# Optimization experiments

Hardware: AMD Instinct MI355X
Metric: run time of the kernel (lower is better)

The kernel has to match this reference:

```python
import jax, jax.numpy as jnp
import numpy as np
import math

NEG_INF = -1e29
B, L, H = 16, 1024, 512
D = 2 * H          # feature dim of s and q
GELU_C = math.sqrt(2.0 / math.pi)


def gelu(x):
    return 0.5 * x * (1.0 + jnp.tanh(GELU_C * (x + 0.044715 * x ** 3)))


def mask_softmax(W, m1, m2):
    # joint mask: [B, len1, 1] * [B, 1, len2]
    m = (m1[:, :, None] * m2[:, None, :]).astype(W.dtype)
    return jax.nn.softmax(W + (1.0 - m) * NEG_INF, axis=-1)


def heuristic(x, y, w_r, b_r, w_g, b_g):
    inp = jnp.concatenate([x, y, x * y, x - y], axis=-1)  # [B, L, 8H]
    r = gelu(inp @ w_r.T + b_r)                           # [B, L, 2H]
    g = jax.nn.sigmoid(inp @ w_g.T + b_g)
    return g * r + (1.0 - g) * x


def setup_inputs() -> dict:
    key = jax.random.key(0)
    k = jax.random.split(key, 6)
    s = jax.random.normal(k[0], (B, L, D), jnp.float32)
    q = jax.random.normal(k[1], (B, L, D), jnp.float32)
    s_mask = jnp.ones((B, L), jnp.int32)
    q_mask = jnp.ones((B, L), jnp.int32)
    fan_in = 8 * H
    lim = 1.0 / np.sqrt(fan_in)
    w_r = jax.random.uniform(k[2], (2 * H, fan_in), jnp.float32, -lim, lim)
    b_r = jax.random.uniform(k[3], (2 * H,), jnp.float32, -lim, lim)
    w_g = jax.random.uniform(k[4], (2 * H, fan_in), jnp.float32, -lim, lim)
    b_g = jax.random.uniform(k[5], (2 * H,), jnp.float32, -lim, lim)
    return {"s": s, "q": q, "w_r": w_r, "b_r": b_r, "w_g": w_g, "b_g": b_g,
            "s_mask": s_mask, "q_mask": q_mask}


def reference(s, q, w_r, b_r, w_g, b_g, s_mask, q_mask):
    a = jnp.einsum('bsd,btd->bst', s, q)                  # [B, Ls, Lq]
    b = mask_softmax(a, s_mask, q_mask) @ q               # [B, Ls, D]
    c = mask_softmax(a.swapaxes(-1, -2), q_mask, s_mask) @ s  # [B, Lq, D]
    s_tilde = heuristic(s, b, w_r, b_r, w_g, b_g)
    q_tilde = heuristic(q, c, w_r, b_r, w_g, b_g)
    return (s_tilde, q_tilde)
```

## Files before the change

kernel.cpp:

```cpp
#include <hip/hip_runtime.h>
#include <hip/hip_bf16.h>
#include <math.h>

#define DEVI static __device__ __forceinline__

typedef unsigned short u16;
typedef unsigned int u32;
typedef __bf16 bf16_t;
typedef bf16_t bf16x8 __attribute__((ext_vector_type(8)));
typedef float f32x4 __attribute__((ext_vector_type(4)));

static constexpr int Bb = 16;
static constexpr int L  = 1024;
static constexpr int D  = 1024;
static constexpr int KH = 4096;

DEVI u16 f2bf(float f) {
  union { float f; u32 u; } v; v.f = f;
  u32 r = v.u + 0x7FFFu + ((v.u >> 16) & 1u);
  return (u16)(r >> 16);
}

DEVI float bf2f(u16 b) {
  union { u32 u; float f; } v; v.u = ((u32)b) << 16;
  return v.f;
}

DEVI void gload16(const void* g, void* l) {
  __builtin_amdgcn_global_load_lds((const __attribute__((address_space(1))) u32*)g,
                                   (__attribute__((address_space(3))) u32*)l,
                                   16, 0, 0);
}

DEVI int swz(int row, int col) { return col ^ ((row & 7) << 3); }

__global__ void k_cast_split(const float* __restrict__ in, u16* __restrict__ hi,
                             u16* __restrict__ lo, int n4) {
  int i = blockIdx.x * blockDim.x + threadIdx.x;
  int stride = gridDim.x * blockDim.x;
  for (; i < n4; i += stride) {
    float4 v = ((const float4*)in)[i];
    ushort4 h, l;
    h.x = f2bf(v.x); h.y = f2bf(v.y); h.z = f2bf(v.z); h.w = f2bf(v.w);
    l.x = f2bf(v.x - bf2f(h.x));
    l.y = f2bf(v.y - bf2f(h.y));
    l.z = f2bf(v.z - bf2f(h.z));
    l.w = f2bf(v.w - bf2f(h.w));
    ((ushort4*)hi)[i] = h;
    ((ushort4*)lo)[i] = l;
  }
}

__global__ void k_wcat(const float* __restrict__ wr, const float* __restrict__ wg,
                       u16* __restrict__ wcat, int n4) {
  int i = blockIdx.x * blockDim.x + threadIdx.x;
  int stride = gridDim.x * blockDim.x;
  for (; i < n4; i += stride) {
    int j = i >> 10;
    int c4 = i & 1023;
    const float* src = ((j & 1) ? wg : wr) + (size_t)(j >> 1) * 4096 + c4 * 4;
    float4 v = *(const float4*)src;
    ushort4 o;
    o.x = f2bf(v.x); o.y = f2bf(v.y); o.z = f2bf(v.z); o.w = f2bf(v.w);
    ((ushort4*)wcat)[i] = o;
  }
}

__global__ void k_feat(const u16* __restrict__ x, const u16* __restrict__ y,
                       u16* __restrict__ xy, u16* __restrict__ xmy, int n8) {
  int i = blockIdx.x * blockDim.x + threadIdx.x;
  int stride = gridDim.x * blockDim.x;
  for (; i < n8; i += stride) {
    bf16x8 xv = ((const bf16x8*)x)[i];
    bf16x8 yv = ((const bf16x8*)y)[i];
    bf16x8 p, d;
    #pragma unroll
    for (int j = 0; j < 8; ++j) {
      float xf = (float)xv[j], yf = (float)yv[j];
      p[j] = (bf16_t)(xf * yf);
      d[j] = (bf16_t)(xf - yf);
    }
    ((bf16x8*)xy)[i] = p;
    ((bf16x8*)xmy)[i] = d;
  }
}

__global__ __launch_bounds__(256)
void k_transpose_bf16(const float* __restrict__ in, u16* __restrict__ out) {
  __shared__ float tile[32][33];
  int b = blockIdx.z;
  int d0 = blockIdx.x * 32;
  int l0 = blockIdx.y * 32;
  const float* ip = in + (size_t)b * L * D;
  u16* op = out + (size_t)b * L * D;
  int tx = threadIdx.x, ty = threadIdx.y;
  #pragma unroll
  for (int j = 0; j < 4; ++j)
    tile[ty + 8 * j][tx] = ip[(size_t)(l0 + ty + 8 * j) * D + d0 + tx];
  __syncthreads();
  #pragma unroll
  for (int j = 0; j < 4; ++j)
    op[(size_t)(d0 + ty + 8 * j) * L + l0 + tx] = f2bf(tile[tx][ty + 8 * j]);
}

template<int OUT_BF16>
__global__ __launch_bounds__(256, 4)
void k_gemm_nt(const u16* __restrict__ A, const u16* __restrict__ Bm, void* __restrict__ Cv,
               int K, int ldc, size_t sA, size_t sB, size_t sC, int tilesN)
{
  __shared__ __align__(16) u16 As[128 * 64];
  __shared__ __align__(16) u16 Bs[128 * 64];
  const int bx = blockIdx.x;
  const int tm = bx / tilesN, tn = bx % tilesN;
  const int b = blockIdx.y;
  const u16* Ap = A + (size_t)b * sA + (size_t)tm * 128 * K;
  const u16* Bp = Bm + (size_t)b * sB + (size_t)tn * 128 * K;
  const int tid = threadIdx.x;
  const int lane = tid & 63, wv = tid >> 6;
  const int wm = wv >> 1, wn = wv & 1;
  const int srow = tid >> 3;
  const int scol = (tid & 7) * 8;
  const int scolswz = swz(srow, scol);
  f32x4 acc[4][4] = {};
  for (int k0 = 0; k0 < K; k0 += 64) {
    #pragma unroll
    for (int i = 0; i < 4; ++i) {
      int row = i * 32 + srow;
      gload16(Ap + (size_t)row * K + k0 + scolswz, &As[row * 64 + scol]);
    }
    #pragma unroll
    for (int i = 0; i < 4; ++i) {
      int row = i * 32 + srow;
      gload16(Bp + (size_t)row * K + k0 + scolswz, &Bs[row * 64 + scol]);
    }
    __syncthreads();
    const int hi8 = (lane >> 4) * 8;
    #pragma unroll
    for (int kk = 0; kk < 64; kk += 32) {
      bf16x8 af[4], bfv[4];
      #pragma unroll
      for (int m = 0; m < 4; ++m) {
        int rr = wm * 64 + m * 16 + (lane & 15);
        af[m] = *(const bf16x8*)&As[rr * 64 + swz(rr, kk + hi8)];
      }
      #pragma unroll
      for (int n = 0; n < 4; ++n) {
        int rr = wn * 64 + n * 16 + (lane & 15);
        bfv[n] = *(const bf16x8*)&Bs[rr * 64 + swz(rr, kk + hi8)];
      }
      #pragma unroll
      for (int m = 0; m < 4; ++m)
        #pragma unroll
        for (int n = 0; n < 4; ++n)
          acc[m][n] = __builtin_amdgcn_mfma_f32_16x16x32_bf16(af[m], bfv[n], acc[m][n], 0, 0, 0);
    }
    __syncthreads();
  }
  const int rb = tm * 128 + wm * 64 + ((lane >> 4) << 2);
  const int cb = tn * 128 + wn * 64 + (lane & 15);
  #pragma unroll
  for (int m = 0; m < 4; ++m)
    #pragma unroll
    for (int n = 0; n < 4; ++n)
      #pragma unroll
      for (int j = 0; j < 4; ++j) {
        int r = rb + m * 16 + j, c = cb + n * 16;
        if (OUT_BF16)
          ((u16*)Cv)[(size_t)b * sC + (size_t)r * ldc + c] = f2bf(acc[m][n][j]);
        else
          ((float*)Cv)[(size_t)b * sC + (size_t)r * ldc + c] = acc[m][n][j];
      }
}

__global__ __launch_bounds__(256, 2)
void k_gemm_nt_split(const u16* __restrict__ Ah, const u16* __restrict__ Al,
                     const u16* __restrict__ Bh, const u16* __restrict__ Bl,
                     float* __restrict__ C, int K, int ldc, size_t sAB, size_t sC, int tilesN)
{
  __shared__ __align__(16) u16 Ahs[128 * 64];
  __shared__ __align__(16) u16 Als[128 * 64];
  __shared__ __align__(16) u16 Bhs[128 * 64];
  __shared__ __align__(16) u16 Bls[128 * 64];
  const int bx = blockIdx.x;
  const int tm = bx / tilesN, tn = bx % tilesN;
  const int b = blockIdx.y;
  const size_t aoff = (size_t)b * sAB + (size_t)tm * 128 * K;
  const size_t boff = (size_t)b * sAB + (size_t)tn * 128 * K;
  const int tid = threadIdx.x;
  const int lane = tid & 63, wv = tid >> 6;
  const int wm = wv >> 1, wn = wv & 1;
  const int srow = tid >> 3;
  const int scol = (tid & 7) * 8;
  const int scolswz = swz(srow, scol);
  f32x4 acc[4][4] = {};
  for (int k0 = 0; k0 < K; k0 += 64) {
    #pragma unroll
    for (int i = 0; i < 4; ++i) {
      int row = i * 32 + srow;
      size_t ga = aoff + (size_t)row * K + k0 + scolswz;
      size_t gb = boff + (size_t)row * K + k0 + scolswz;
      int ls = row * 64 + scol;
      gload16(Ah + ga, &Ahs[ls]);
      gload16(Al + ga, &Als[ls]);
      gload16(Bh + gb, &Bhs[ls]);
      gload16(Bl + gb, &Bls[ls]);
    }
    __syncthreads();
    const int hi8 = (lane >> 4) * 8;
    #pragma unroll
    for (int kk = 0; kk < 64; kk += 32) {
      bf16x8 ah[4], al[4], bh[4], bl[4];
      #pragma unroll
      for (int m = 0; m < 4; ++m) {
        int rr = wm * 64 + m * 16 + (lane & 15);
        int off = rr * 64 + swz(rr, kk + hi8);
        ah[m] = *(const bf16x8*)&Ahs[off];
        al[m] = *(const bf16x8*)&Als[off];
      }
      #pragma unroll
      for (int n = 0; n < 4; ++n) {
        int rr = wn * 64 + n * 16 + (lane & 15);
        int off = rr * 64 + swz(rr, kk + hi8);
        bh[n] = *(const bf16x8*)&Bhs[off];
        bl[n] = *(const bf16x8*)&Bls[off];
      }
      #pragma unroll
      for (int m = 0; m < 4; ++m)
        #pragma unroll
        for (int n = 0; n < 4; ++n) {
          acc[m][n] = __builtin_amdgcn_mfma_f32_16x16x32_bf16(ah[m], bh[n], acc[m][n], 0, 0, 0);
          acc[m][n] = __builtin_amdgcn_mfma_f32_16x16x32_bf16(ah[m], bl[n], acc[m][n], 0, 0, 0);
          acc[m][n] = __builtin_amdgcn_mfma_f32_16x16x32_bf16(al[m], bh[n], acc[m][n], 0, 0, 0);
        }
    }
    __syncthreads();
  }
  const int rb = tm * 128 + wm * 64 + ((lane >> 4) << 2);
  const int cb = tn * 128 + wn * 64 + (lane & 15);
  #pragma unroll
  for (int m = 0; m < 4; ++m)
    #pragma unroll
    for (int n = 0; n < 4; ++n)
      #pragma unroll
      for (int j = 0; j < 4; ++j) {
        int r = rb + m * 16 + j, c = cb + n * 16;
        C[(size_t)b * sC + (size_t)r * ldc + c] = acc[m][n][j];
      }
}

__global__ __launch_bounds__(256)
void k_row_softmax(const float* __restrict__ a, u16* __restrict__ P,
                   const int* __restrict__ m1, const int* __restrict__ m2)
{
  const int row = blockIdx.x, b = blockIdx.y;
  const float* ar = a + ((size_t)b * L + row) * L;
  const int tid = threadIdx.x, lane = tid & 63, wv = tid >> 6;
  __shared__ float redm[4], reds[4];
  float4 v = ((const float4*)ar)[tid];
  int4 mv = ((const int4*)(m2 + (size_t)b * L))[tid];
  const int mr = m1[(size_t)b * L + row];
  float x0 = v.x + (float)(1 - mr * mv.x) * (-1e29f);
  float x1 = v.y + (float)(1 - mr * mv.y) * (-1e29f);
  float x2 = v.z + (float)(1 - mr * mv.z) * (-1e29f);
  float x3 = v.w + (float)(1 - mr * mv.w) * (-1e29f);
  float mx = fmaxf(fmaxf(x0, x1), fmaxf(x2, x3));
  #pragma unroll
  for (int o = 32; o > 0; o >>= 1) mx = fmaxf(mx, __shfl_xor(mx, o));
  if (lane == 0) redm[wv] = mx;
  __syncthreads();
  mx = fmaxf(fmaxf(redm[0], redm[1]), fmaxf(redm[2], redm[3]));
  float e0 = __expf(x0 - mx), e1 = __expf(x1 - mx), e2 = __expf(x2 - mx), e3 = __expf(x3 - mx);
  float s4 = e0 + e1 + e2 + e3;
  #pragma unroll
  for (int o = 32; o > 0; o >>= 1) s4 += __shfl_xor(s4, o);
  if (lane == 0) reds[wv] = s4;
  __syncthreads();
  float inv = 1.0f / (reds[0] + reds[1] + reds[2] + reds[3]);
  ushort4 o;
  o.x = f2bf(e0 * inv); o.y = f2bf(e1 * inv); o.z = f2bf(e2 * inv); o.w = f2bf(e3 * inv);
  ((ushort4*)(P + ((size_t)b * L + row) * L))[tid] = o;
}

__global__ __launch_bounds__(256)
void k_col_softmax(const float* __restrict__ a, u16* __restrict__ P,
                   const int* __restrict__ mrow, const int* __restrict__ mcol)
{
  __shared__ float mred[4][64], lred[4][64];
  __shared__ float Mc[64], Li[64];
  __shared__ u16 T[64][68];
  const int b = blockIdx.y;
  const int c0 = blockIdx.x * 64;
  const int tid = threadIdx.x;
  const int cl = tid & 63;
  const int qr = tid >> 6;
  const int c = c0 + cl;
  const float* ab = a + (size_t)b * L * L;
  const int mc = mcol[(size_t)b * L + c];
  const int* msk = mrow + (size_t)b * L;
  float m = -3.0e38f, l = 0.0f;
  for (int r = qr * 256; r < qr * 256 + 256; ++r) {
    float x = ab[(size_t)r * L + c] + (float)(1 - mc * msk[r]) * (-1e29f);
    float mn = fmaxf(m, x);
    l = l * __expf(m - mn) + __expf(x - mn);
    m = mn;
  }
  mred[qr][cl] = m; lred[qr][cl] = l;
  __syncthreads();
  if (tid < 64) {
    float M = fmaxf(fmaxf(mred[0][tid], mred[1][tid]), fmaxf(mred[2][tid], mred[3][tid]));
    float Lt = lred[0][tid] * __expf(mred[0][tid] - M) + lred[1][tid] * __expf(mred[1][tid] - M)
             + lred[2][tid] * __expf(mred[2][tid] - M) + lred[3][tid] * __expf(mred[3][tid] - M);
    Mc[tid] = M; Li[tid] = 1.0f / Lt;
  }
  __syncthreads();
  const float M = Mc[cl], Linv = Li[cl];
  u16* Pb = P + (size_t)b * L * L;
  const int tl = tid >> 2, sc = (tid & 3) * 16;
  for (int ch = 0; ch < 16; ++ch) {
    #pragma unroll
    for (int rs = 0; rs < 16; ++rs) {
      int r = ch * 64 + qr * 16 + rs;
      float x = ab[(size_t)r * L + c] + (float)(1 - mc * msk[r]) * (-1e29f);
      T[cl][qr * 16 + rs] = f2bf(__expf(x - M) * Linv);
    }
    __syncthreads();
    ushort4* d4 = (ushort4*)(Pb + (size_t)(c0 + tl) * L + ch * 64 + sc);
    #pragma unroll
    for (int jj = 0; jj < 4; ++jj) {
      ushort4 v;
      v.x = T[tl][sc + jj * 4 + 0]; v.y = T[tl][sc + jj * 4 + 1];
      v.z = T[tl][sc + jj * 4 + 2]; v.w = T[tl][sc + jj * 4 + 3];
      d4[jj] = v;
    }
    __syncthreads();
  }
}

__global__ __launch_bounds__(256, 4)
void k_heur5(const u16* __restrict__ X, const u16* __restrict__ Y,
             const u16* __restrict__ XY, const u16* __restrict__ XMY,
             const u16* __restrict__ Wc,
             const float* __restrict__ br, const float* __restrict__ bg,
             const float* __restrict__ Xf, float* __restrict__ out)
{
  __shared__ __align__(16) u16 As[128 * 64];
  __shared__ __align__(16) u16 Bs[128 * 64];
  const int bx = blockIdx.x;
  const int xcd = bx & 7, li = bx >> 3;
  const int tn = li & 15, tm = xcd * 16 + (li >> 4);
  const size_t rowBase = (size_t)tm * 128;
  const int colBase = tn * 128;
  const u16* Bp = Wc + (size_t)colBase * KH;
  const int tid = threadIdx.x;
  const int lane = tid & 63, wv = tid >> 6;
  const int wm = wv >> 1, wn = wv & 1;
  const int srow = tid >> 3;
  const int scol = (tid & 7) * 8;
  const int scolswz = swz(srow, scol);
  f32x4 acc[4][4] = {};
  for (int k0 = 0; k0 < KH; k0 += 64) {
    const u16* ap = (k0 < 2048) ? (k0 < 1024 ? X : Y) : (k0 < 3072 ? XY : XMY);
    const int kc = k0 & 1023;
    #pragma unroll
    for (int i = 0; i < 4; ++i) {
      int row = i * 32 + srow;
      gload16(ap + (rowBase + row) * (size_t)D + kc + scolswz, &As[row * 64 + scol]);
    }
    #pragma unroll
    for (int i = 0; i < 4; ++i) {
      int row = i * 32 + srow;
      gload16(Bp + (size_t)row * KH + k0 + scolswz, &Bs[row * 64 + scol]);
    }
    __syncthreads();
    const int hi8 = (lane >> 4) * 8;
    #pragma unroll
    for (int kk = 0; kk < 64; kk += 32) {
      bf16x8 af[4], bfv[4];
      #pragma unroll
      for (int m = 0; m < 4; ++m) {
        int rr = wm * 64 + m * 16 + (lane & 15);
        af[m] = *(const bf16x8*)&As[rr * 64 + swz(rr, kk + hi8)];
      }
      #pragma unroll
      for (int n = 0; n < 4; ++n) {
        int rr = wn * 64 + n * 16 + (lane & 15);
        bfv[n] = *(const bf16x8*)&Bs[rr * 64 + swz(rr, kk + hi8)];
      }
      #pragma unroll
      for (int m = 0; m < 4; ++m)
        #pragma unroll
        for (int n = 0; n < 4; ++n)
          acc[m][n] = __builtin_amdgcn_mfma_f32_16x16x32_bf16(af[m], bfv[n], acc[m][n], 0, 0, 0);
    }
    __syncthreads();
  }
  const int rb = wm * 64 + ((lane >> 4) << 2);
  const int cbl = wn * 64 + (lane & 15);
  const int odd = lane & 1;
  #pragma unroll
  for (int m = 0; m < 4; ++m)
    #pragma unroll
    for (int n = 0; n < 4; ++n) {
      int ncol = colBase + cbl + n * 16;
      int cc = ncol >> 1;
      #pragma unroll
      for (int j = 0; j < 4; ++j) {
        size_t row = rowBase + rb + m * 16 + j;
        float v = acc[m][n][j];
        float pv = __shfl_xor(v, 1);
        float r = odd ? pv : v;
        float g = odd ? v : pv;
        r += br[cc]; g += bg[cc];
        float th = tanhf(0.79788456080286535588f * (r + 0.044715f * r * r * r));
        float gl = 0.5f * r * (1.0f + th);
        float sg = 1.0f / (1.0f + __expf(-g));
        float xv = Xf[row * (size_t)D + cc];
        float res = sg * gl + (1.0f - sg) * xv;
        if (!odd) out[row * (size_t)D + cc] = res;
      }
    }
}

extern "C" void kernel_launch(void* const* d_in, const int* in_sizes, int n_in,
                              void* d_out, int out_size, void* d_ws, size_t ws_size,
                              hipStream_t stream)
{
  (void)in_sizes; (void)n_in; (void)out_size; (void)ws_size;
  const float* s    = (const float*)d_in[0];
  const float* q    = (const float*)d_in[1];
  const float* w_r  = (const float*)d_in[2];
  const float* b_r  = (const float*)d_in[3];
  const float* w_g  = (const float*)d_in[4];
  const float* b_g  = (const float*)d_in[5];
  const int* s_mask = (const int*)d_in[6];
  const int* q_mask = (const int*)d_in[7];
  float* out = (float*)d_out;

  const size_t SQ = (size_t)Bb * L * D;
  const size_t W  = (size_t)D * KH;
  const size_t S1 = (size_t)L * D;

  char* p = (char*)d_ws;
  u16* s_bf  = (u16*)p; p += SQ * 2;
  u16* q_bf  = (u16*)p; p += SQ * 2;
  u16* buf1  = (u16*)p; p += SQ * 2;
  u16* buf2  = (u16*)p; p += SQ * 2;
  u16* b_bf  = (u16*)p; p += SQ * 2;
  u16* c_bf  = (u16*)p; p += SQ * 2;
  u16* wcat  = (u16*)p; p += 2 * W * 2;

  float* a  = out;
  u16*   P1 = (u16*)(out + SQ);
  u16*   P2 = (u16*)(out + SQ + SQ / 2);

  dim3 blk(256);
  k_cast_split<<<4096, blk, 0, stream>>>(s, s_bf, buf1, (int)(SQ / 4));
  k_cast_split<<<4096, blk, 0, stream>>>(q, q_bf, buf2, (int)(SQ / 4));
  k_wcat<<<4096, blk, 0, stream>>>(w_r, w_g, wcat, (int)(2 * W / 4));

  dim3 ggrid(64, Bb);
  k_gemm_nt_split<<<ggrid, blk, 0, stream>>>(s_bf, buf1, q_bf, buf2, a, D, L, S1, (size_t)L * L, 8);
  k_row_softmax<<<dim3(L, Bb), blk, 0, stream>>>(a, P1, s_mask, q_mask);
  k_col_softmax<<<dim3(L / 64, Bb), blk, 0, stream>>>(a, P2, s_mask, q_mask);

  dim3 tgrid(D / 32, L / 32, Bb), tblk(32, 8);
  k_transpose_bf16<<<tgrid, tblk, 0, stream>>>(s, buf1);
  k_transpose_bf16<<<tgrid, tblk, 0, stream>>>(q, buf2);

  k_gemm_nt<1><<<ggrid, blk, 0, stream>>>(P1, buf2, b_bf, L, D, (size_t)L * L, S1, S1, 8);
  k_gemm_nt<1><<<ggrid, blk, 0, stream>>>(P2, buf1, c_bf, L, D, (size_t)L * L, S1, S1, 8);

  k_feat<<<2048, blk, 0, stream>>>(s_bf, b_bf, buf1, buf2, (int)(SQ / 8));
  k_heur5<<<2048, blk, 0, stream>>>(s_bf, b_bf, buf1, buf2, wcat, b_r, b_g, s, out);

  k_feat<<<2048, blk, 0, stream>>>(q_bf, c_bf, buf1, buf2, (int)(SQ / 8));
  k_heur5<<<2048, blk, 0, stream>>>(q_bf, c_bf, buf1, buf2, wcat, b_r, b_g, q, out + SQ);
}
```

Measured before the change: 1.062 ms.

## Double-buffer LDS in score and heuristic GEMMs with K=32 stages

The split-precision score GEMM and the heuristic GEMM now prefetch the next K=32 slice into a second LDS buffer while computing the current one, with one barrier per step. The score GEMM no longer loads four operand tiles per step. It walks three K segments (hi·hi, hi·lo, lo·hi), each a plain bf16 GEMM. This cuts LDS use and allows occupancy 4 instead of 2, so global-load latency can hide behind MFMA work. In exchange there are twice as many barriers per unit of K, and a new XOR swizzle for the 32-wide rows.

New measurement: 1.248 ms. 1.18x slower.

```diff
diff --git a/kernel.cpp b/kernel.cpp
--- a/kernel.cpp
+++ b/kernel.cpp
@@ -172,67 +172,59 @@
       }
 }
 
-__global__ __launch_bounds__(256, 2)
-void k_gemm_nt_split(const u16* __restrict__ Ah, const u16* __restrict__ Al,
-                     const u16* __restrict__ Bh, const u16* __restrict__ Bl,
-                     float* __restrict__ C, int K, int ldc, size_t sAB, size_t sC, int tilesN)
-{
-  __shared__ __align__(16) u16 Ahs[128 * 64];
-  __shared__ __align__(16) u16 Als[128 * 64];
-  __shared__ __align__(16) u16 Bhs[128 * 64];
-  __shared__ __align__(16) u16 Bls[128 * 64];
-  const int bx = blockIdx.x;
-  const int tm = bx / tilesN, tn = bx % tilesN;
-  const int b = blockIdx.y;
-  const size_t aoff = (size_t)b * sAB + (size_t)tm * 128 * K;
-  const size_t boff = (size_t)b * sAB + (size_t)tn * 128 * K;
-  const int tid = threadIdx.x;
-  const int lane = tid & 63, wv = tid >> 6;
+__global__ __launch_bounds__(256, 4)
+void k_scores(const u16* __restrict__ Ah, const u16* __restrict__ Al,
+              const u16* __restrict__ Bh, const u16* __restrict__ Bl,
+              float* __restrict__ C)
+{
+  __shared__ __align__(16) u16 As[2][128 * 32];
+  __shared__ __align__(16) u16 Bs[2][128 * 32];
+  const int bx = blockIdx.x, b = blockIdx.y;
+  const int tm = bx >> 3, tn = bx & 7;
+  const size_t S1 = (size_t)L * D;
+  const size_t abase = (size_t)b * S1 + (size_t)tm * 128 * D;
+  const size_t bbase = (size_t)b * S1 + (size_t)tn * 128 * D;
+  const int tid = threadIdx.x, lane = tid & 63, wv = tid >> 6;
   const int wm = wv >> 1, wn = wv & 1;
-  const int srow = tid >> 3;
-  const int scol = (tid & 7) * 8;
-  const int scolswz = swz(srow, scol);
   f32x4 acc[4][4] = {};
-  for (int k0 = 0; k0 < K; k0 += 64) {
-    #pragma unroll
-    for (int i = 0; i < 4; ++i) {
-      int row = i * 32 + srow;
-      size_t ga = aoff + (size_t)row * K + k0 + scolswz;
-      size_t gb = boff + (size_t)row * K + k0 + scolswz;
-      int ls = row * 64 + scol;
-      gload16(Ah + ga, &Ahs[ls]);
-      gload16(Al + ga, &Als[ls]);
-      gload16(Bh + gb, &Bhs[ls]);
-      gload16(Bl + gb, &Bls[ls]);
-    }
-    __syncthreads();
-    const int hi8 = (lane >> 4) * 8;
-    #pragma unroll
-    for (int kk = 0; kk < 64; kk += 32) {
-      bf16x8 ah[4], al[4], bh[4], bl[4];
-      #pragma unroll
-      for (int m = 0; m < 4; ++m) {
-        int rr = wm * 64 + m * 16 + (lane & 15);
-        int off = rr * 64 + swz(rr, kk + hi8);
-        ah[m] = *(const bf16x8*)&Ahs[off];
-        al[m] = *(const bf16x8*)&Als[off];
-      }
-      #pragma unroll
-      for (int n = 0; n < 4; ++n) {
-        int rr = wn * 64 + n * 16 + (lane & 15);
-        int off = rr * 64 + swz(rr, kk + hi8);
-        bh[n] = *(const bf16x8*)&Bhs[off];
-        bl[n] = *(const bf16x8*)&Bls[off];
-      }
-      #pragma unroll
-      for (int m = 0; m < 4; ++m)
-        #pragma unroll
-        for (int n = 0; n < 4; ++n) {
-          acc[m][n] = __builtin_amdgcn_mfma_f32_16x16x32_bf16(ah[m], bh[n], acc[m][n], 0, 0, 0);
-          acc[m][n] = __builtin_amdgcn_mfma_f32_16x16x32_bf16(ah[m], bl[n], acc[m][n], 0, 0, 0);
-          acc[m][n] = __builtin_amdgcn_mfma_f32_16x16x32_bf16(al[m], bh[n], acc[m][n], 0, 0, 0);
-        }
-    }
+
+  auto stage = [&](int t, int buf) {
+    const int seg = t >> 5;
+    const u16* ap = (seg == 2) ? Al : Ah;
+    const u16* bp = (seg == 1) ? Bl : Bh;
+    const int kc = (t & 31) * 32;
+    #pragma unroll
+    for (int j = 0; j < 2; ++j) {
+      int s = j * 256 + tid;
+      int row = s >> 2, sp = s & 3;
+      int csrc = (sp ^ ((row >> 1) & 3)) * 8;
+      gload16(ap + abase + (size_t)row * D + kc + csrc, &As[buf][s * 8]);
+      gload16(bp + bbase + (size_t)row * D + kc + csrc, &Bs[buf][s * 8]);
+    }
+  };
+
+  stage(0, 0);
+  __syncthreads();
+  for (int t = 0; t < 96; ++t) {
+    const int cur = t & 1;
+    if (t < 95) stage(t + 1, cur ^ 1);
+    const int g = lane >> 4, l15 = lane & 15;
+    bf16x8 af[4], bfv[4];
+    #pragma unroll
+    for (int m = 0; m < 4; ++m) {
+      int rr = wm * 64 + m * 16 + l15;
+      af[m] = *(const bf16x8*)&As[cur][(rr * 4 + (g ^ ((rr >> 1) & 3))) * 8];
+    }
+    #pragma unroll
+    for (int n = 0; n < 4; ++n) {
+      int rr = wn * 64 + n * 16 + l15;
+      bfv[n] = *(const bf16x8*)&Bs[cur][(rr * 4 + (g ^ ((rr >> 1) & 3))) * 8];
+    }
+    #pragma unroll
+    for (int m = 0; m < 4; ++m)
+      #pragma unroll
+      for (int n = 0; n < 4; ++n)
+        acc[m][n] = __builtin_amdgcn_mfma_f32_16x16x32_bf16(af[m], bfv[n], acc[m][n], 0, 0, 0);
     __syncthreads();
   }
   const int rb = tm * 128 + wm * 64 + ((lane >> 4) << 2);
@@ -242,10 +234,8 @@
     #pragma unroll
     for (int n = 0; n < 4; ++n)
       #pragma unroll
-      for (int j = 0; j < 4; ++j) {
-        int r = rb + m * 16 + j, c = cb + n * 16;
-        C[(size_t)b * sC + (size_t)r * ldc + c] = acc[m][n][j];
-      }
+      for (int j = 0; j < 4; ++j)
+        C[(size_t)b * L * L + (size_t)(rb + m * 16 + j) * L + cb + n * 16] = acc[m][n][j];
 }
 
 __global__ __launch_bounds__(256)
@@ -337,63 +327,63 @@
 }
 
 __global__ __launch_bounds__(256, 4)
-void k_heur5(const u16* __restrict__ X, const u16* __restrict__ Y,
+void k_heur6(const u16* __restrict__ X, const u16* __restrict__ Y,
              const u16* __restrict__ XY, const u16* __restrict__ XMY,
              const u16* __restrict__ Wc,
              const float* __restrict__ br, const float* __restrict__ bg,
              const float* __restrict__ Xf, float* __restrict__ out)
 {
-  __shared__ __align__(16) u16 As[128 * 64];
-  __shared__ __align__(16) u16 Bs[128 * 64];
+  __shared__ __align__(16) u16 As[2][128 * 32];
+  __shared__ __align__(16) u16 Bs[2][128 * 32];
   const int bx = blockIdx.x;
   const int xcd = bx & 7, li = bx >> 3;
   const int tn = li & 15, tm = xcd * 16 + (li >> 4);
   const size_t rowBase = (size_t)tm * 128;
   const int colBase = tn * 128;
-  const u16* Bp = Wc + (size_t)colBase * KH;
-  const int tid = threadIdx.x;
-  const int lane = tid & 63, wv = tid >> 6;
+  const int tid = threadIdx.x, lane = tid & 63, wv = tid >> 6;
   const int wm = wv >> 1, wn = wv & 1;
-  const int srow = tid >> 3;
-  const int scol = (tid & 7) * 8;
-  const int scolswz = swz(srow, scol);
   f32x4 acc[4][4] = {};
-  for (int k0 = 0; k0 < KH; k0 += 64) {
-    const u16* ap = (k0 < 2048) ? (k0 < 1024 ? X : Y) : (k0 < 3072 ? XY : XMY);
-    const int kc = k0 & 1023;
-    #pragma unroll
-    for (int i = 0; i < 4; ++i) {
-      int row = i * 32 + srow;
-      gload16(ap + (rowBase + row) * (size_t)D + kc + scolswz, &As[row * 64 + scol]);
-    }
-    #pragma unroll
-    for (int i = 0; i < 4; ++i) {
-      int row = i * 32 + srow;
-      gload16(Bp + (size_t)row * KH + k0 + scolswz, &Bs[row * 64 + scol]);
-    }
-    __syncthreads();
-    const int hi8 = (lane >> 4) * 8;
-    #pragma unroll
-    for (int kk = 0; kk < 64; kk += 32) {
-      bf16x8 af[4], bfv[4];
-      #pragma unroll
-      for (int m = 0; m < 4; ++m) {
-        int rr = wm * 64 + m * 16 + (lane & 15);
-        af[m] = *(const bf16x8*)&As[rr * 64 + swz(rr, kk + hi8)];
-      }
-      #pragma unroll
-      for (int n = 0; n < 4; ++n) {
-        int rr = wn * 64 + n * 16 + (lane & 15);
-        bfv[n] = *(const bf16x8*)&Bs[rr * 64 + swz(rr, kk + hi8)];
-      }
-      #pragma unroll
-      for (int m = 0; m < 4; ++m)
-        #pragma unroll
-        for (int n = 0; n < 4; ++n)
-          acc[m][n] = __builtin_amdgcn_mfma_f32_16x16x32_bf16(af[m], bfv[n], acc[m][n], 0, 0, 0);
-    }
-    __syncthreads();
-  }
+
+  auto stage = [&](int t, int buf) {
+    const int fa = t >> 5;
+    const u16* ap = (fa == 0) ? X : (fa == 1) ? Y : (fa == 2) ? XY : XMY;
+    const int kc = (t & 31) * 32;
+    const int kw = t * 32;
+    #pragma unroll
+    for (int j = 0; j < 2; ++j) {
+      int s = j * 256 + tid;
+      int row = s >> 2, sp = s & 3;
+      int csrc = (sp ^ ((row >> 1) & 3)) * 8;
+      gload16(ap + (rowBase + row) * (size_t)D + kc + csrc, &As[buf][s * 8]);
+      gload16(Wc + (size_t)(colBase + row) * KH + kw + csrc, &Bs[buf][s * 8]);
+    }
+  };
+
+  stage(0, 0);
+  __syncthreads();
+  for (int t = 0; t < 128; ++t) {
+    const int cur = t & 1;
+    if (t < 127) stage(t + 1, cur ^ 1);
+    const int g = lane >> 4, l15 = lane & 15;
+    bf16x8 af[4], bfv[4];
+    #pragma unroll
+    for (int m = 0; m < 4; ++m) {
+      int rr = wm * 64 + m * 16 + l15;
+      af[m] = *(const bf16x8*)&As[cur][(rr * 4 + (g ^ ((rr >> 1) & 3))) * 8];
+    }
+    #pragma unroll
+    for (int n = 0; n < 4; ++n) {
+      int rr = wn * 64 + n * 16 + l15;
+      bfv[n] = *(const bf16x8*)&Bs[cur][(rr * 4 + (g ^ ((rr >> 1) & 3))) * 8];
+    }
+    #pragma unroll
+    for (int m = 0; m < 4; ++m)
+      #pragma unroll
+      for (int n = 0; n < 4; ++n)
+        acc[m][n] = __builtin_amdgcn_mfma_f32_16x16x32_bf16(af[m], bfv[n], acc[m][n], 0, 0, 0);
+    __syncthreads();
+  }
+
   const int rb = wm * 64 + ((lane >> 4) << 2);
   const int cbl = wn * 64 + (lane & 15);
   const int odd = lane & 1;
@@ -409,11 +399,11 @@
         float v = acc[m][n][j];
         float pv = __shfl_xor(v, 1);
         float r = odd ? pv : v;
-        float g = odd ? v : pv;
-        r += br[cc]; g += bg[cc];
+        float g2 = odd ? v : pv;
+        r += br[cc]; g2 += bg[cc];
         float th = tanhf(0.79788456080286535588f * (r + 0.044715f * r * r * r));
         float gl = 0.5f * r * (1.0f + th);
-        float sg = 1.0f / (1.0f + __expf(-g));
+        float sg = 1.0f / (1.0f + __expf(-g2));
         float xv = Xf[row * (size_t)D + cc];
         float res = sg * gl + (1.0f - sg) * xv;
         if (!odd) out[row * (size_t)D + cc] = res;
@@ -458,8 +448,7 @@
   k_cast_split<<<4096, blk, 0, stream>>>(q, q_bf, buf2, (int)(SQ / 4));
   k_wcat<<<4096, blk, 0, stream>>>(w_r, w_g, wcat, (int)(2 * W / 4));
 
-  dim3 ggrid(64, Bb);
-  k_gemm_nt_split<<<ggrid, blk, 0, stream>>>(s_bf, buf1, q_bf, buf2, a, D, L, S1, (size_t)L * L, 8);
+  k_scores<<<dim3(64, Bb), blk, 0, stream>>>(s_bf, buf1, q_bf, buf2, a);
   k_row_softmax<<<dim3(L, Bb), blk, 0, stream>>>(a, P1, s_mask, q_mask);
   k_col_softmax<<<dim3(L / 64, Bb), blk, 0, stream>>>(a, P2, s_mask, q_mask);
 
@@ -467,12 +456,13 @@
   k_transpose_bf16<<<tgrid, tblk, 0, stream>>>(s, buf1);
   k_transpose_bf16<<<tgrid, tblk, 0, stream>>>(q, buf2);
 
+  dim3 ggrid(64, Bb);
   k_gemm_nt<1><<<ggrid, blk, 0, stream>>>(P1, buf2, b_bf, L, D, (size_t)L * L, S1, S1, 8);
   k_gemm_nt<1><<<ggrid, blk, 0, stream>>>(P2, buf1, c_bf, L, D, (size_t)L * L, S1, S1, 8);
 
   k_feat<<<2048, blk, 0, stream>>>(s_bf, b_bf, buf1, buf2, (int)(SQ / 8));
-  k_heur5<<<2048, blk, 0, stream>>>(s_bf, b_bf, buf1, buf2, wcat, b_r, b_g, s, out);
+  k_heur6<<<2048, blk, 0, stream>>>(s_bf, b_bf, buf1, buf2, wcat, b_r, b_g, s, out);
 
   k_feat<<<2048, blk, 0, stream>>>(q_bf, c_bf, buf1, buf2, (int)(SQ / 8));
-  k_heur5<<<2048, blk, 0, stream>>>(q_bf, c_bf, buf1, buf2, wcat, b_r, b_g, q, out + SQ);
-}
+  k_heur6<<<2048, blk, 0, stream>>>(q_bf, c_bf, buf1, buf2, wcat, b_r, b_g, q, out + SQ);
+}
```
